# Kernel optimization log

Measured on AMD Instinct MI355X. Metric: run time of the kernel, lower is better.

## Reference

```python
import jax, jax.numpy as jnp
import numpy as np

B, D, N, H = 2, 1024, 2048, 16
DH = D // H  # head dim 64


def setup_inputs() -> dict:
    key = jax.random.key(0)
    ks = jax.random.split(key, 10)
    query = jax.random.normal(ks[0], (B, D, N), jnp.float32)
    att_mask = jax.random.randint(ks[1], (B, 1, N), 0, 2).astype(bool)
    w = lambda k: jax.random.normal(k, (D, D), jnp.float32) * 0.02
    b = lambda k: jax.random.normal(k, (D,), jnp.float32) * 0.02
    return dict(
        query=query,
        Wq=w(ks[2]), bq=b(ks[3]),
        Wk=w(ks[4]), bk=b(ks[5]),
        Wv=w(ks[6]), bv=b(ks[7]),
        Wo=w(ks[8]), bo=b(ks[9]),
        att_mask=att_mask,
    )


def _proj(W, bias, x):  # conv1d k=1: [B,D,N] -> [B,D,N]
    return jnp.einsum('ed,bdn->ben', W, x) + bias[None, :, None]


def _split_heads(t):  # [B,N,D] -> [B*H,N,DH], batch-major flatten
    return t.reshape(B, N, H, DH).transpose(0, 2, 1, 3).reshape(B * H, N, DH)


def _attention(q, k, v, att_mask):
    scale = 1.0 / np.sqrt(DH)
    att = jnp.einsum('bqd,bkd->bqk', q * scale, k)  # [B*H,N,N]
    # faithful to original: mask repeated along q_len then tiled num_heads times on dim 0
    m = jnp.tile(jnp.broadcast_to(att_mask, (B, N, N)), (H, 1, 1))
    att = jnp.where(m, att, -jnp.inf)
    fully_masked = ~m.any(axis=(-2, -1))  # [B*H]
    att = jnp.where(fully_masked[:, None, None], 1e-5, att)
    p = jax.nn.softmax(att, axis=-1)
    y = jnp.einsum('bqk,bkd->bqd', p, v)
    return y * (~fully_masked).astype(y.dtype)[:, None, None]


def reference(query, Wq, bq, Wk, bk, Wv, bv, Wo, bo, att_mask):
    # projections (Conv1d kernel_size=1 == channel-dim linear)
    q = _split_heads(_proj(Wq, bq, query).transpose(0, 2, 1))
    k = _split_heads(_proj(Wk, bk, query).transpose(0, 2, 1))
    v = _split_heads(_proj(Wv, bv, query).transpose(0, 2, 1))
    y = _attention(q, k, v, att_mask)  # [B*H,N,DH]
    # combine heads -> [B,N,D] -> channels-first [B,D,N]
    z = y.reshape(B, H, N, DH).transpose(0, 2, 1, 3).reshape(B, N, D).transpose(0, 2, 1)
    # output projection (dropouts are identity in eval mode)
    return _proj(Wo, bo, z)
```

## Files before the change

### kernel.cpp

```cpp
#include <hip/hip_runtime.h>
#include <hip/hip_bf16.h>

#define BATCH 2
#define DMODEL 1024
#define SEQ 2048
#define NHEAD 16
#define DHEAD 64
#define BH (BATCH*NHEAD)
#define COLS (BATCH*SEQ)

typedef __attribute__((ext_vector_type(8))) short bf16x8;
typedef __attribute__((ext_vector_type(4))) float f32x4;
typedef __attribute__((ext_vector_type(16))) float f32x16;

__device__ inline unsigned short f2bf(float f) {
    unsigned u = __builtin_bit_cast(unsigned, f);
    unsigned r = (u + 0x7FFFu + ((u >> 16) & 1u)) >> 16;
    return (unsigned short)r;
}

__device__ inline f32x4 mfma16(bf16x8 a, bf16x8 b, f32x4 c) {
    return __builtin_amdgcn_mfma_f32_16x16x32_bf16(a, b, c, 0, 0, 0);
}
__device__ inline f32x16 mfma32(bf16x8 a, bf16x8 b, f32x16 c) {
    return __builtin_amdgcn_mfma_f32_32x32x16_bf16(a, b, c, 0, 0, 0);
}

__device__ __forceinline__ void gload_lds16(const unsigned short* g, unsigned short* l) {
    __builtin_amdgcn_global_load_lds(
        (const __attribute__((address_space(1))) unsigned int*)g,
        (__attribute__((address_space(3))) unsigned int*)l, 16, 0, 0);
}

__device__ inline unsigned cvtpk(float lo, float hi) {
    unsigned r;
    asm("v_cvt_pk_bf16_f32 %0, %1, %2" : "=v"(r) : "v"(lo), "v"(hi));
    return r;
}
__device__ inline float fexp2(float x) {
    float r;
    asm("v_exp_f32 %0, %1" : "=v"(r) : "v"(x));
    return r;
}

__global__ __launch_bounds__(256) void cvt_w(
    const float* __restrict__ w0, const float* __restrict__ w1,
    const float* __restrict__ w2, const float* __restrict__ w3,
    unsigned short* __restrict__ out)
{
    int which = blockIdx.y;
    const float* src = (which == 0) ? w0 : (which == 1) ? w1 : (which == 2) ? w2 : w3;
    size_t base = (size_t)which * (DMODEL * DMODEL);
    size_t i = ((size_t)blockIdx.x * 256 + threadIdx.x) * 4;
    float4 v = *(const float4*)&src[i];
    ushort4 o;
    o.x = f2bf(v.x); o.y = f2bf(v.y); o.z = f2bf(v.z); o.w = f2bf(v.w);
    *(ushort4*)&out[base + i] = o;
}

__global__ __launch_bounds__(64) void prep_mask(
    const int* __restrict__ mask, unsigned long long* __restrict__ mw,
    unsigned short* __restrict__ maskvb)
{
    int lane = threadIdx.x;
    int tile = blockIdx.x;
    int mb = tile >> 5, tt = tile & 31;
    int mv = mask[mb * SEQ + tt * 64 + lane];
    unsigned long long bits = __ballot(mv != 0);
    if (lane == 0) mw[tile] = bits;
    int q2 = (lane >> 2) & 3;
    int q2s = ((q2 & 1) << 1) | (q2 >> 1);
    int pp = (lane & ~15) | (q2s << 2) | (lane & 3);
    maskvb[mb * SEQ + tt * 64 + pp] = mv ? 0x3F80 : 0;
}

__global__ __launch_bounds__(256) void transpose_q(
    const float* __restrict__ q, unsigned short* __restrict__ Xt)
{
    __shared__ float tile[32][33];
    int b = blockIdx.z;
    int d0 = blockIdx.y * 32, n0 = blockIdx.x * 32;
    int tx = threadIdx.x, ty = threadIdx.y;
#pragma unroll
    for (int i = 0; i < 32; i += 8)
        tile[ty + i][tx] = q[(size_t)b * DMODEL * SEQ + (size_t)(d0 + ty + i) * SEQ + n0 + tx];
    __syncthreads();
#pragma unroll
    for (int i = 0; i < 32; i += 8)
        Xt[(size_t)b * SEQ * DMODEL + (size_t)(n0 + ty + i) * DMODEL + d0 + tx] = f2bf(tile[tx][ty + i]);
}

__global__ __launch_bounds__(256) void gemm_qkv(
    const unsigned short* __restrict__ Xt,
    const unsigned short* __restrict__ W3,
    const float* __restrict__ bq, const float* __restrict__ bk, const float* __restrict__ bv,
    const int* __restrict__ mask,
    unsigned short* __restrict__ Qb, unsigned short* __restrict__ Kbuf,
    unsigned short* __restrict__ Vtb)
{
    const int K = DMODEL;
    __shared__ unsigned short sA[128 * 32];
    __shared__ unsigned short sB[128 * 32];
    int t = threadIdx.x, lane = t & 63, w = t >> 6;
    int wr = w >> 1, wc = w & 1;
    int tt0 = blockIdx.y * 128;
    int ct0 = blockIdx.x * 128;
    int mat = ct0 >> 10, ec0 = ct0 & 1023;
    const float* bs = (mat == 0) ? bq : (mat == 1) ? bk : bv;
    int rl = lane & 15, ko = (lane >> 4) << 3;
    int srow = lane >> 2, scol = (lane & 3) << 3;

    f32x4 acc[4][4] = {};
    for (int kb = 0; kb < K; kb += 32) {
        __syncthreads();
        gload_lds16(&Xt[(size_t)(tt0 + w * 32 + srow) * K + kb + scol],      &sA[(w * 32) * 32]);
        gload_lds16(&Xt[(size_t)(tt0 + w * 32 + 16 + srow) * K + kb + scol], &sA[(w * 32 + 16) * 32]);
        gload_lds16(&W3[(size_t)(ct0 + w * 32 + srow) * K + kb + scol],      &sB[(w * 32) * 32]);
        gload_lds16(&W3[(size_t)(ct0 + w * 32 + 16 + srow) * K + kb + scol], &sB[(w * 32 + 16) * 32]);
        __syncthreads();
        bf16x8 af[4], bfr[4];
#pragma unroll
        for (int m = 0; m < 4; m++)
            af[m] = *(const bf16x8*)&sA[(wr * 64 + m * 16 + rl) * 32 + ko];
#pragma unroll
        for (int n = 0; n < 4; n++)
            bfr[n] = *(const bf16x8*)&sB[(wc * 64 + n * 16 + rl) * 32 + ko];
#pragma unroll
        for (int m = 0; m < 4; m++)
#pragma unroll
            for (int n = 0; n < 4; n++)
                acc[m][n] = mfma16(af[m], bfr[n], acc[m][n]);
    }

    const float QS = 0.125f;
    int rowb = (lane >> 4) * 4, col = lane & 15;
#pragma unroll
    for (int m = 0; m < 4; m++) {
#pragma unroll
        for (int n = 0; n < 4; n++) {
            int ee = ec0 + wc * 64 + n * 16 + col;
            int hh = ee >> 6, dd = ee & 63;
            float bias = bs[ee];
#pragma unroll
            for (int r = 0; r < 4; r++) {
                int tk = tt0 + wr * 64 + m * 16 + rowb + r;
                int b = tk >> 11, nn = tk & (SEQ - 1);
                float v = acc[m][n][r] + bias;
                if (mat == 0) {
                    v *= QS;
                    Qb[((size_t)(b * NHEAD + hh) * SEQ + nn) * DHEAD + dd] = f2bf(v);
                } else if (mat == 1) {
                    Kbuf[((size_t)(b * NHEAD + hh) * SEQ + nn) * DHEAD + dd] = f2bf(v);
                } else {
                    if (mask[(hh & 1) * SEQ + nn] == 0) v = 0.f;
                    int q2 = (nn >> 2) & 3;
                    int q2s = ((q2 & 1) << 1) | (q2 >> 1);
                    int np = (nn & ~15) | (q2s << 2) | (nn & 3);
                    int tl = np >> 6, kk = np & 63;
                    int ks = kk >> 4, hi2 = (kk >> 3) & 1, jj = kk & 7;
                    Vtb[((((size_t)(b * NHEAD + hh) * 32 + tl) * 8 + ks * 2 + hi2) * 64 + dd) * 8 + jj] = f2bf(v);
                }
            }
        }
    }
}

__global__ __launch_bounds__(256) void gemm_out(
    const unsigned short* __restrict__ A,
    const unsigned short* __restrict__ Bt,
    const float* __restrict__ bias,
    float* __restrict__ outf)
{
    const int K = DMODEL;
    __shared__ unsigned short sA[128 * 32];
    __shared__ unsigned short sB[64 * 32];
    int t = threadIdx.x, lane = t & 63, w = t >> 6;
    int wr = w >> 1, wc = w & 1;
    int et0 = blockIdx.y * 128, ct0 = blockIdx.x * 64;
    int rl = lane & 15, ko = (lane >> 4) << 3;
    int srow = lane >> 2, scol = (lane & 3) << 3;

    f32x4 acc[4][2] = {};
    for (int kb = 0; kb < K; kb += 32) {
        __syncthreads();
        gload_lds16(&A[(size_t)(et0 + w * 16 + srow) * K + kb + scol],      &sA[(w * 16) * 32]);
        gload_lds16(&A[(size_t)(et0 + 64 + w * 16 + srow) * K + kb + scol], &sA[(64 + w * 16) * 32]);
        gload_lds16(&Bt[(size_t)(ct0 + w * 16 + srow) * K + kb + scol],     &sB[(w * 16) * 32]);
        __syncthreads();
        bf16x8 af[4], bfr[2];
#pragma unroll
        for (int m = 0; m < 4; m++)
            af[m] = *(const bf16x8*)&sA[(wr * 64 + m * 16 + rl) * 32 + ko];
#pragma unroll
        for (int n = 0; n < 2; n++)
            bfr[n] = *(const bf16x8*)&sB[(wc * 32 + n * 16 + rl) * 32 + ko];
#pragma unroll
        for (int m = 0; m < 4; m++)
#pragma unroll
            for (int n = 0; n < 2; n++)
                acc[m][n] = mfma16(af[m], bfr[n], acc[m][n]);
    }

    int rowb = (lane >> 4) * 4, col = lane & 15;
#pragma unroll
    for (int m = 0; m < 4; m++) {
#pragma unroll
        for (int n = 0; n < 2; n++) {
            int c = ct0 + wc * 32 + n * 16 + col;
            int b = c >> 11, nn = c & (SEQ - 1);
#pragma unroll
            for (int r = 0; r < 4; r++) {
                int e = et0 + wr * 64 + m * 16 + rowb + r;
                outf[((size_t)b * DMODEL + e) * SEQ + nn] = acc[m][n][r] + bias[e];
            }
        }
    }
}

__global__ __launch_bounds__(256, 2) void attn(
    const unsigned short* __restrict__ Q,
    const unsigned short* __restrict__ Kb,
    const unsigned short* __restrict__ Vt,
    const unsigned long long* __restrict__ mwords,
    const unsigned short* __restrict__ maskvb,
    unsigned short* __restrict__ Zt)
{
    __shared__ unsigned short sK[2][64 * 64];

    int bid = blockIdx.x;
    int xcd = bid & 7, slot = bid >> 3;
    int bh = xcd + 8 * (slot >> 4);
    int qb = slot & 15;
    int b = bh >> 4, h = bh & 15;
    int mb = bh & (BATCH - 1);
    int t = threadIdx.x, lane = t & 63, w = t >> 6;
    int hi = lane >> 5, ql = lane & 31;
    int q0 = qb * 128 + w * 32;
    const unsigned short* Qp = Q + (size_t)bh * SEQ * DHEAD;
    const unsigned short* Kp = Kb + (size_t)bh * SEQ * DHEAD;
    const unsigned short* Vg = Vt + (size_t)bh * SEQ * DHEAD;
    const unsigned long long* mw = mwords + mb * 32;
    const unsigned short* Mv = maskvb + mb * SEQ;

    int srow0 = w * 16 + (lane >> 3);
    int ssw   = ((lane & 7) ^ ((lane >> 3) & 7)) << 3;

    unsigned long long anyb = 0ull;
#pragma unroll
    for (int i = 0; i < 32; i++) anyb |= mw[i];

    bf16x8 qf[4];
#pragma unroll
    for (int c = 0; c < 4; c++)
        qf[c] = *(const bf16x8*)&Qp[(size_t)(q0 + ql) * DHEAD + c * 16 + hi * 8];

    f32x16 Y0 = {}, Y1 = {}, Yl = {};
    float m_ = -1e30f;
    const float LOG2E = 1.442695041f;

    int rsw = ql & 7;

    gload_lds16(&Kp[(size_t)srow0 * DHEAD + ssw],       &sK[0][(w * 16) * 64]);
    gload_lds16(&Kp[(size_t)(srow0 + 8) * DHEAD + ssw], &sK[0][(w * 16 + 8) * 64]);
    __syncthreads();

    for (int tt0 = 0; tt0 < 32; tt0++) {
        int cur = tt0 & 1;
        if (tt0 < 31) {
            int kn = (tt0 + 1) * 64;
            gload_lds16(&Kp[(size_t)(kn + srow0) * DHEAD + ssw],     &sK[cur ^ 1][(w * 16) * 64]);
            gload_lds16(&Kp[(size_t)(kn + srow0 + 8) * DHEAD + ssw], &sK[cur ^ 1][(w * 16 + 8) * 64]);
        }

        const unsigned short* vt = &Vg[(size_t)tt0 * 4096];
        bf16x8 vb0[4], vb1[4], im[4];
#pragma unroll
        for (int ks = 0; ks < 4; ks++) {
            vb0[ks] = *(const bf16x8*)&vt[(size_t)((ks * 2 + hi) * 64 + ql) * 8];
            vb1[ks] = *(const bf16x8*)&vt[(size_t)((ks * 2 + hi) * 64 + 32 + ql) * 8];
            im[ks]  = *(const bf16x8*)&Mv[tt0 * 64 + 16 * ks + 8 * hi];
        }

        f32x16 S0 = {}, S1 = {};
        __builtin_amdgcn_s_setprio(1);
#pragma unroll
        for (int c = 0; c < 4; c++) {
            bf16x8 kf = *(const bf16x8*)&sK[cur][ql * 64 + ((((c << 1) | hi) ^ rsw) << 3)];
            S0 = mfma32(kf, qf[c], S0);
        }
#pragma unroll
        for (int c = 0; c < 4; c++) {
            bf16x8 kf = *(const bf16x8*)&sK[cur][(32 + ql) * 64 + ((((c << 1) | hi) ^ rsw) << 3)];
            S1 = mfma32(kf, qf[c], S1);
        }
        __builtin_amdgcn_s_setprio(0);

        float t0[16];
#pragma unroll
        for (int r = 0; r < 16; r++) t0[r] = fmaxf(S0[r], S1[r]);
#pragma unroll
        for (int s = 8; s > 0; s >>= 1)
#pragma unroll
            for (int r = 0; r < 8; r++)
                if (r < s) t0[r] = fmaxf(t0[r], t0[r + s]);
        float pmax = fmaxf(t0[0], __shfl_xor(t0[0], 32, 64));

        float mnew = fmaxf(m_, pmax);
        if (!__all(pmax <= m_ + 8.0f)) {
            float al = __expf(m_ - mnew);
            m_ = mnew;
#pragma unroll
            for (int reg = 0; reg < 16; reg++) {
                float av = __shfl(al, (reg & 3) + 8 * (reg >> 2) + 4 * hi, 64);
                Y0[reg] *= av;
                Y1[reg] *= av;
                Yl[reg] *= av;
            }
        }

        float nmL = -m_ * LOG2E;
        float p[32];
#pragma unroll
        for (int rr = 0; rr < 16; rr++) p[rr] = fexp2(fmaf(S0[rr], LOG2E, nmL));
#pragma unroll
        for (int rr = 0; rr < 16; rr++) p[16 + rr] = fexp2(fmaf(S1[rr], LOG2E, nmL));

        unsigned PKa[8], PKb[8];
#pragma unroll
        for (int i = 0; i < 8; i++) {
            PKa[i] = cvtpk(p[4 * i], p[4 * i + 1]);
            PKb[i] = cvtpk(p[4 * i + 2], p[4 * i + 3]);
        }

        bf16x8 pa[4];
#pragma unroll
        for (int ks = 0; ks < 4; ks++) {
            union { unsigned u[4]; bf16x8 v; } pu;
            pu.u[0] = PKa[2 * ks];
            pu.u[1] = PKb[2 * ks];
            pu.u[2] = PKa[2 * ks + 1];
            pu.u[3] = PKb[2 * ks + 1];
            pa[ks] = pu.v;
        }

        __builtin_amdgcn_s_setprio(1);
#pragma unroll
        for (int ks = 0; ks < 4; ks++) {
            Y0 = mfma32(pa[ks], vb0[ks], Y0);
            Y1 = mfma32(pa[ks], vb1[ks], Y1);
            Yl = mfma32(pa[ks], im[ks],  Yl);
        }
        __builtin_amdgcn_s_setprio(0);

        __syncthreads();
    }

#pragma unroll
    for (int reg = 0; reg < 16; reg++) {
        float lv = (anyb != 0ull) ? (1.0f / Yl[reg]) : 0.f;
        int row = (reg & 3) + 8 * (reg >> 2) + 4 * hi;
        int n = q0 + row;
        size_t base = ((size_t)b * SEQ + n) * DMODEL + h * DHEAD;
        Zt[base + ql] = f2bf(Y0[reg] * lv);
        Zt[base + 32 + ql] = f2bf(Y1[reg] * lv);
    }
}

extern "C" void kernel_launch(void* const* d_in, const int* in_sizes, int n_in,
                              void* d_out, int out_size, void* d_ws, size_t ws_size,
                              hipStream_t stream) {
    const float* query = (const float*)d_in[0];
    const float* Wq = (const float*)d_in[1];
    const float* bq = (const float*)d_in[2];
    const float* Wk = (const float*)d_in[3];
    const float* bk = (const float*)d_in[4];
    const float* Wv = (const float*)d_in[5];
    const float* bv = (const float*)d_in[6];
    const float* Wo = (const float*)d_in[7];
    const float* bo = (const float*)d_in[8];
    const int* mask = (const int*)d_in[9];
    float* out = (float*)d_out;

    char* ws = (char*)d_ws;
    unsigned short* Wb  = (unsigned short*)(ws);
    unsigned short* Xt  = (unsigned short*)(ws + ((size_t)8  << 20));
    unsigned short* Qb  = (unsigned short*)(ws + ((size_t)16 << 20));
    unsigned short* Kbuf= (unsigned short*)(ws + ((size_t)24 << 20));
    unsigned short* Vtb = (unsigned short*)(ws + ((size_t)32 << 20));
    unsigned short* Zt  = (unsigned short*)(ws + ((size_t)40 << 20));
    unsigned long long* mwords = (unsigned long long*)(ws + ((size_t)48 << 20));
    unsigned short* maskvb = (unsigned short*)(ws + ((size_t)48 << 20) + 65536);

    const size_t WSZ = (size_t)DMODEL * DMODEL;

    cvt_w<<<dim3(DMODEL * DMODEL / 1024, 4), 256, 0, stream>>>(Wq, Wk, Wv, Wo, Wb);
    prep_mask<<<64, 64, 0, stream>>>(mask, mwords, maskvb);
    transpose_q<<<dim3(SEQ / 32, DMODEL / 32, BATCH), dim3(32, 8), 0, stream>>>(query, Xt);

    gemm_qkv<<<dim3(3 * DMODEL / 128, COLS / 128), 256, 0, stream>>>(
        Xt, Wb, bq, bk, bv, mask, Qb, Kbuf, Vtb);

    attn<<<512, 256, 0, stream>>>(Qb, Kbuf, Vtb, mwords, maskvb, Zt);

    gemm_out<<<dim3(COLS / 64, DMODEL / 128), 256, 0, stream>>>(
        Wb + 3 * WSZ, Zt, bo, out);
}
```

Baseline: 137.3 us.

## Split attention KV range across two wave groups and merge partial softmax

```diff
diff --git a/kernel.cpp b/kernel.cpp
--- a/kernel.cpp
+++ b/kernel.cpp
@@ -217,7 +217,7 @@
     }
 }
 
-__global__ __launch_bounds__(256, 2) void attn(
+__global__ __launch_bounds__(512) void attn(
     const unsigned short* __restrict__ Q,
     const unsigned short* __restrict__ Kb,
     const unsigned short* __restrict__ Vt,
@@ -225,7 +225,9 @@
     const unsigned short* __restrict__ maskvb,
     unsigned short* __restrict__ Zt)
 {
-    __shared__ unsigned short sK[2][64 * 64];
+    __shared__ __align__(16) char smem[50176];
+    unsigned short* sK = (unsigned short*)smem;
+    float* mg = (float*)smem;
 
     int bid = blockIdx.x;
     int xcd = bid & 7, slot = bid >> 3;
@@ -234,15 +236,18 @@
     int b = bh >> 4, h = bh & 15;
     int mb = bh & (BATCH - 1);
     int t = threadIdx.x, lane = t & 63, w = t >> 6;
+    int qw = w & 3, kh = w >> 2;
     int hi = lane >> 5, ql = lane & 31;
-    int q0 = qb * 128 + w * 32;
+    int q0 = qb * 128 + qw * 32;
     const unsigned short* Qp = Q + (size_t)bh * SEQ * DHEAD;
     const unsigned short* Kp = Kb + (size_t)bh * SEQ * DHEAD;
     const unsigned short* Vg = Vt + (size_t)bh * SEQ * DHEAD;
     const unsigned long long* mw = mwords + mb * 32;
     const unsigned short* Mv = maskvb + mb * SEQ;
 
-    int srow0 = w * 16 + (lane >> 3);
+    unsigned short* sKh = sK + (kh * 2) * 4096;
+
+    int srow0 = qw * 16 + (lane >> 3);
     int ssw   = ((lane & 7) ^ ((lane >> 3) & 7)) << 3;
 
     unsigned long long anyb = 0ull;
@@ -257,40 +262,41 @@
     f32x16 Y0 = {}, Y1 = {}, Yl = {};
     float m_ = -1e30f;
     const float LOG2E = 1.442695041f;
-
     int rsw = ql & 7;
-
-    gload_lds16(&Kp[(size_t)srow0 * DHEAD + ssw],       &sK[0][(w * 16) * 64]);
-    gload_lds16(&Kp[(size_t)(srow0 + 8) * DHEAD + ssw], &sK[0][(w * 16 + 8) * 64]);
+    int kbase = kh * 1024;
+
+    gload_lds16(&Kp[(size_t)(kbase + srow0) * DHEAD + ssw],       &sKh[(qw * 16) * 64]);
+    gload_lds16(&Kp[(size_t)(kbase + srow0 + 8) * DHEAD + ssw],   &sKh[(qw * 16 + 8) * 64]);
     __syncthreads();
 
-    for (int tt0 = 0; tt0 < 32; tt0++) {
-        int cur = tt0 & 1;
-        if (tt0 < 31) {
-            int kn = (tt0 + 1) * 64;
-            gload_lds16(&Kp[(size_t)(kn + srow0) * DHEAD + ssw],     &sK[cur ^ 1][(w * 16) * 64]);
-            gload_lds16(&Kp[(size_t)(kn + srow0 + 8) * DHEAD + ssw], &sK[cur ^ 1][(w * 16 + 8) * 64]);
-        }
-
-        const unsigned short* vt = &Vg[(size_t)tt0 * 4096];
+    for (int tt = 0; tt < 16; tt++) {
+        int cur = tt & 1;
+        int atile = kh * 16 + tt;
+        if (tt < 15) {
+            int kn = (atile + 1) * 64;
+            gload_lds16(&Kp[(size_t)(kn + srow0) * DHEAD + ssw],     &sKh[(cur ^ 1) * 4096 + (qw * 16) * 64]);
+            gload_lds16(&Kp[(size_t)(kn + srow0 + 8) * DHEAD + ssw], &sKh[(cur ^ 1) * 4096 + (qw * 16 + 8) * 64]);
+        }
+
+        const unsigned short* vt = &Vg[(size_t)atile * 4096];
         bf16x8 vb0[4], vb1[4], im[4];
 #pragma unroll
         for (int ks = 0; ks < 4; ks++) {
             vb0[ks] = *(const bf16x8*)&vt[(size_t)((ks * 2 + hi) * 64 + ql) * 8];
             vb1[ks] = *(const bf16x8*)&vt[(size_t)((ks * 2 + hi) * 64 + 32 + ql) * 8];
-            im[ks]  = *(const bf16x8*)&Mv[tt0 * 64 + 16 * ks + 8 * hi];
+            im[ks]  = *(const bf16x8*)&Mv[atile * 64 + 16 * ks + 8 * hi];
         }
 
         f32x16 S0 = {}, S1 = {};
         __builtin_amdgcn_s_setprio(1);
 #pragma unroll
         for (int c = 0; c < 4; c++) {
-            bf16x8 kf = *(const bf16x8*)&sK[cur][ql * 64 + ((((c << 1) | hi) ^ rsw) << 3)];
+            bf16x8 kf = *(const bf16x8*)&sKh[cur * 4096 + ql * 64 + ((((c << 1) | hi) ^ rsw) << 3)];
             S0 = mfma32(kf, qf[c], S0);
         }
 #pragma unroll
         for (int c = 0; c < 4; c++) {
-            bf16x8 kf = *(const bf16x8*)&sK[cur][(32 + ql) * 64 + ((((c << 1) | hi) ^ rsw) << 3)];
+            bf16x8 kf = *(const bf16x8*)&sKh[cur * 4096 + (32 + ql) * 64 + ((((c << 1) | hi) ^ rsw) << 3)];
             S1 = mfma32(kf, qf[c], S1);
         }
         __builtin_amdgcn_s_setprio(0);
@@ -303,10 +309,10 @@
 #pragma unroll
             for (int r = 0; r < 8; r++)
                 if (r < s) t0[r] = fmaxf(t0[r], t0[r + s]);
-        float pmax = fmaxf(t0[0], __shfl_xor(t0[0], 32, 64));
-
-        float mnew = fmaxf(m_, pmax);
-        if (!__all(pmax <= m_ + 8.0f)) {
+
+        if (!__all(t0[0] <= m_ + 8.0f)) {
+            float pmax = fmaxf(t0[0], __shfl_xor(t0[0], 32, 64));
+            float mnew = fmaxf(m_, pmax);
             float al = __expf(m_ - mnew);
             m_ = mnew;
 #pragma unroll
@@ -355,14 +361,35 @@
         __syncthreads();
     }
 
-#pragma unroll
-    for (int reg = 0; reg < 16; reg++) {
-        float lv = (anyb != 0ull) ? (1.0f / Yl[reg]) : 0.f;
-        int row = (reg & 3) + 8 * (reg >> 2) + 4 * hi;
-        int n = q0 + row;
-        size_t base = ((size_t)b * SEQ + n) * DMODEL + h * DHEAD;
-        Zt[base + ql] = f2bf(Y0[reg] * lv);
-        Zt[base + 32 + ql] = f2bf(Y1[reg] * lv);
+    float* myq = mg + ((size_t)qw * 64 + lane) * 49;
+    if (kh == 1) {
+#pragma unroll
+        for (int reg = 0; reg < 16; reg++) {
+            myq[reg] = Y0[reg];
+            myq[16 + reg] = Y1[reg];
+            myq[32 + reg] = Yl[reg];
+        }
+        myq[48] = m_;
+    }
+    __syncthreads();
+    if (kh == 0) {
+        float mB = myq[48];
+        float ms = fmaxf(m_, mB);
+        float aA = __expf(m_ - ms), aB = __expf(mB - ms);
+#pragma unroll
+        for (int reg = 0; reg < 16; reg++) {
+            int row = (reg & 3) + 8 * (reg >> 2) + 4 * hi;
+            float aAv = __shfl(aA, row, 64);
+            float aBv = __shfl(aB, row, 64);
+            float y0 = Y0[reg] * aAv + myq[reg] * aBv;
+            float y1 = Y1[reg] * aAv + myq[16 + reg] * aBv;
+            float yl = Yl[reg] * aAv + myq[32 + reg] * aBv;
+            float lv = (anyb != 0ull) ? (1.0f / yl) : 0.f;
+            int n = q0 + row;
+            size_t base = ((size_t)b * SEQ + n) * DMODEL + h * DHEAD;
+            Zt[base + ql] = f2bf(y0 * lv);
+            Zt[base + 32 + ql] = f2bf(y1 * lv);
+        }
     }
 }
 
@@ -400,7 +427,7 @@
     gemm_qkv<<<dim3(3 * DMODEL / 128, COLS / 128), 256, 0, stream>>>(
         Xt, Wb, bq, bk, bv, mask, Qb, Kbuf, Vtb);
 
-    attn<<<512, 256, 0, stream>>>(Qb, Kbuf, Vtb, mwords, maskvb, Zt);
+    attn<<<512, 512, 0, stream>>>(Qb, Kbuf, Vtb, mwords, maskvb, Zt);
 
     gemm_out<<<dim3(COLS / 64, DMODEL / 128), 256, 0, stream>>>(
         Wb + 3 * WSZ, Zt, bo, out);
```

Result: slower. 140.2 us (+2.1%).
